# Performance work log

Measured on AMD Instinct MI355X. Metric: run time of the kernel, lower is better.

## Reference

```python
import jax, jax.numpy as jnp
import numpy as np

AUTHOR_FAMILY_CODET = jnp.array([0, 1, 2, 1, 3, 3], dtype=jnp.int32)
MARGIN = 0.3

def setup_inputs() -> dict:
    key = jax.random.key(0)
    k1, k2 = jax.random.split(key)
    B, D = 8192, 256
    embeddings = jax.random.normal(k1, (B, D), dtype=jnp.float32)
    labels = jax.random.randint(k2, (B,), 0, 6, dtype=jnp.int64)
    return {"embeddings": embeddings, "labels": labels}

def reference(embeddings, labels):
    B = embeddings.shape[0]
    # family lookup; labels out of table range would be -1 (cannot happen here
    # since fill_max == table length, but kept for faithfulness)
    lab = labels.astype(jnp.int32)
    table_len = AUTHOR_FAMILY_CODET.shape[0]
    fam = jnp.where(lab < table_len,
                    AUTHOR_FAMILY_CODET[jnp.clip(lab, 0, table_len - 1)],
                    -1)
    # cosine distance matrix [B, B]
    emb_norm = embeddings / jnp.linalg.norm(embeddings, axis=-1, keepdims=True)
    dist = 1.0 - emb_norm @ emb_norm.T
    valid_row = fam >= 0                                   # [B]
    same = (fam[:, None] == fam[None, :]) & valid_row[:, None]
    same = same & ~jnp.eye(B, dtype=bool)                  # exclude self
    diff = (fam[:, None] != fam[None, :]) & valid_row[None, :] & valid_row[:, None]
    d_pos = jnp.max(jnp.where(same, dist, -2.0), axis=1)   # hardest positive
    d_neg = jnp.min(jnp.where(diff, dist, 4.0), axis=1)    # hardest negative
    valid = valid_row & jnp.any(same, axis=1) & jnp.any(diff, axis=1)
    triplet = jax.nn.relu(d_pos - d_neg + MARGIN) * valid.astype(dist.dtype)
    count = jnp.sum(valid.astype(jnp.int32))
    return jnp.sum(triplet) / jnp.maximum(count, 1).astype(dist.dtype)
```

## Files before the change

kernel.cpp:

```cpp
#include <hip/hip_runtime.h>


typedef __attribute__((ext_vector_type(8))) _Float16 half8;
typedef __attribute__((ext_vector_type(2))) _Float16 half2v;
typedef __attribute__((ext_vector_type(4))) float floatx4;
typedef __attribute__((ext_vector_type(4))) unsigned short ushort4v;

constexpr int DIN = 256;
constexpr int NKS = 9;
constexpr int TILE_USH = NKS * 4 * 64 * 8;
#define MARGIN 0.3f
#define FAM_PACKED 111240
#define SENT 0xC4004400u

static __device__ __forceinline__ unsigned fkey(float x) {
  return __builtin_bit_cast(unsigned, x + 10.0f);
}
static __device__ __forceinline__ unsigned packmm(float mn, float mx) {
  unsigned lo = __builtin_bit_cast(unsigned short, (_Float16)mn);
  unsigned hi = __builtin_bit_cast(unsigned short, (_Float16)mx);
  return lo | (hi << 16);
}
static __device__ __forceinline__ float mmlo(unsigned p) {
  return (float)__builtin_bit_cast(_Float16, (unsigned short)(p & 0xFFFF));
}
static __device__ __forceinline__ float mmhi(unsigned p) {
  return (float)__builtin_bit_cast(_Float16, (unsigned short)(p >> 16));
}
static __device__ __forceinline__ unsigned pkmin(unsigned a, unsigned b) {
  half2v x = __builtin_bit_cast(half2v, a);
  half2v y = __builtin_bit_cast(half2v, b);
  return __builtin_bit_cast(unsigned, __builtin_elementwise_min(x, y));
}

static __device__ __forceinline__ void ld_g2l16(const unsigned short* g,
                                                unsigned short* lds) {
  __builtin_amdgcn_global_load_lds(
      (const __attribute__((address_space(1))) unsigned int*)(const void*)g,
      (__attribute__((address_space(3))) unsigned int*)(void*)lds, 16, 0, 0);
}

__global__ __launch_bounds__(256) void prep_kernel(
    const float* __restrict__ E, const int* __restrict__ labels,
    unsigned short* __restrict__ EhB, unsigned* __restrict__ mnK,
    unsigned* __restrict__ mxK, float* __restrict__ sumAcc,
    int* __restrict__ cntAcc, int* __restrict__ doneCnt, int B) {
  if (blockIdx.x == 0 && threadIdx.x == 0) {
    sumAcc[0] = 0.0f; cntAcc[0] = 0; doneCnt[0] = 0;
  }
  int gid = blockIdx.x * 256 + threadIdx.x;
  if (gid < B) { mnK[gid] = 0xFFFFFFFFu; mxK[gid] = 0u; }
  int wave = blockIdx.x * 4 + (threadIdx.x >> 6);
  int lane = threadIdx.x & 63;
  int nw   = gridDim.x * 4;
  const int ksl = lane >> 3, ql = (lane >> 1) & 3, ol = (lane & 1) * 4;
  for (int row = wave; row < B; row += nw) {
    float4 v = *(const float4*)&E[(long)row * DIN + lane * 4];
    float s = v.x * v.x + v.y * v.y + v.z * v.z + v.w * v.w;
#pragma unroll
    for (int o = 1; o < 64; o <<= 1) s += __shfl_xor(s, o);
    float rn = 1.0f / sqrtf(s);
    ushort4v o4;
    o4.x = __builtin_bit_cast(unsigned short, (_Float16)(v.x * rn));
    o4.y = __builtin_bit_cast(unsigned short, (_Float16)(v.y * rn));
    o4.z = __builtin_bit_cast(unsigned short, (_Float16)(v.z * rn));
    o4.w = __builtin_bit_cast(unsigned short, (_Float16)(v.w * rn));
    const int ct = row >> 6, nj = (row >> 4) & 3, mrow = row & 15;
    const long tbase = (long)ct * TILE_USH;
    *(ushort4v*)&EhB[tbase + ((long)(ksl * 4 + nj) * 64 + ql * 16 + mrow) * 8
                     + ol] = o4;
    if (lane < 8) {
      ushort4v z = {0, 0, 0, 0};
      if (lane == 0) {
        int lab = labels[row];
        int labc = lab < 0 ? 0 : (lab > 5 ? 5 : lab);
        int fm = (FAM_PACKED >> (3 * labc)) & 7;
        z.x = fm == 0 ? 0x4400 : 0;
        z.y = fm == 1 ? 0x4400 : 0;
        z.z = fm == 2 ? 0x4400 : 0;
        z.w = fm == 3 ? 0x4400 : 0;
      }
      *(ushort4v*)&EhB[tbase + ((long)(8 * 4 + nj) * 64 + ql * 16 + mrow) * 8
                       + ol] = z;
    }
  }
}

__global__ __launch_bounds__(256, 2) void gram_kernel(
    const unsigned short* __restrict__ EhB, unsigned* __restrict__ mnK,
    unsigned* __restrict__ mxK, int nt, int nTasks) {
  __shared__ unsigned short Bs[2][TILE_USH];
  __shared__ unsigned colS[2][4][64];

  const int w = threadIdx.x >> 6, l = threadIdx.x & 63;
  const int m = l & 15, q = l >> 4;

  const int nwg = gridDim.x;
  const int bid = (int)blockIdx.x;
  const int swz = (bid & 7) * (nwg >> 3) + (bid >> 3);

  const int t0 = (int)(((long)swz * nTasks) / nwg);
  const int t1 = (int)(((long)(swz + 1) * nTasks) / nwg);

  int rb = 0;
  while ((rb + 1) * (nt - rb) <= t0) ++rb;
  int ct = 2 * rb + (t0 - rb * (nt - rb + 1));

  const unsigned short* baseL = EhB + l * 8;

  auto stage = [&](int buf, int ctv) {
    const unsigned short* src =
        EhB + (long)ctv * TILE_USH + (long)(w * 64 + l) * 8;
    unsigned short* dst = &Bs[buf][(w * 64) * 8];
#pragma unroll
    for (int j = 0; j < 9; ++j)
      ld_g2l16(src + j * 2048, dst + j * 2048);
  };

  half8 apan[NKS][2];
  auto loadA = [&](int rbv) {
    const long at = (long)(2 * rbv + (w >> 1)) * TILE_USH;
#pragma unroll
    for (int ks = 0; ks < NKS; ++ks)
#pragma unroll
      for (int mi = 0; mi < 2; ++mi)
        apan[ks][mi] = *(const half8*)
            &baseL[at + (long)(ks * 4 + (w & 1) * 2 + mi) * 512];
    apan[8][0] = apan[8][0] * (_Float16)-0.5f;
    apan[8][1] = apan[8][1] * (_Float16)-0.5f;
  };
  loadA(rb);

  float rAmn[8], rAmx[8];
  bool any = false;
#pragma unroll
  for (int i = 0; i < 8; ++i) { rAmn[i] = 100.0f; rAmx[i] = -100.0f; }

  auto flushRows = [&](int rbv) {
    if (!any) return;
#pragma unroll
    for (int o = 1; o < 16; o <<= 1)
#pragma unroll
      for (int i = 0; i < 8; ++i) {
        rAmn[i] = fminf(rAmn[i], __shfl_xor(rAmn[i], o));
        rAmx[i] = fmaxf(rAmx[i], __shfl_xor(rAmx[i], o));
      }
    if (m == 0) {
      const int r0 = rbv * 128 + w * 32 + q * 4;
#pragma unroll
      for (int mi = 0; mi < 2; ++mi)
#pragma unroll
        for (int r = 0; r < 4; ++r) {
          int row = r0 + mi * 16 + r;
          atomicMin(&mnK[row], fkey(rAmn[mi * 4 + r]));
          atomicMax(&mxK[row], fkey(rAmx[mi * 4 + r]));
        }
    }
  };

  auto mergeCols = [&](int pct, int sb2) {
    if (l >= 16) return;
    unsigned a = SENT ^ 0x80000000u;
#pragma unroll
    for (int ww = 0; ww < 4; ++ww)
      a = pkmin(a, colS[sb2][ww][w * 16 + l] ^ 0x80000000u);
    a ^= 0x80000000u;
    float mn = mmlo(a), mx = mmhi(a);
    int col = pct * 64 + w * 16 + l;
    if (mn < 3.9f) atomicMin(&mnK[col], fkey(mn));
    if (mx > -3.9f) atomicMax(&mxK[col], fkey(mx));
  };

  stage(0, ct);
  int p = 0, pct = -1;

#pragma unroll 1
  for (int f = t0; f < t1; ++f) {
    __syncthreads();

    int nct = ct + 1, nrb = rb;
    if (nct == nt) { ++nrb; nct = 2 * nrb; }
    if (f + 1 < t1) stage(p ^ 1, nct);

    if (pct >= 0) mergeCols(pct, (f - 1) & 1);

    const int rt64 = 2 * rb + (w >> 1);
    const int sb = f & 1;
    if (rt64 <= ct) {
      any = true;
      floatx4 acc[2][4];
#pragma unroll
      for (int mi = 0; mi < 2; ++mi)
#pragma unroll
        for (int nj = 0; nj < 4; ++nj) acc[mi][nj] = (floatx4)0.0f;
#pragma unroll
      for (int ks = 0; ks < NKS; ++ks) {
        half8 b[4];
#pragma unroll
        for (int nj = 0; nj < 4; ++nj)
          b[nj] = *(const half8*)&Bs[p][((ks * 4 + nj) * 64 + l) * 8];
#pragma unroll
        for (int mi = 0; mi < 2; ++mi)
#pragma unroll
          for (int nj = 0; nj < 4; ++nj)
            acc[mi][nj] = __builtin_amdgcn_mfma_f32_16x16x32_f16(
                apan[ks][mi], b[nj], acc[mi][nj], 0, 0, 0);
      }
      float cMn[4], cMx[4];
#pragma unroll
      for (int nj = 0; nj < 4; ++nj) {
        float a0 = fminf(fminf(acc[0][nj][0], acc[0][nj][1]),
                         fminf(acc[0][nj][2], acc[0][nj][3]));
        float a1 = fminf(fminf(acc[1][nj][0], acc[1][nj][1]),
                         fminf(acc[1][nj][2], acc[1][nj][3]));
        float b0 = fmaxf(fmaxf(acc[0][nj][0], acc[0][nj][1]),
                         fmaxf(acc[0][nj][2], acc[0][nj][3]));
        float b1 = fmaxf(fmaxf(acc[1][nj][0], acc[1][nj][1]),
                         fmaxf(acc[1][nj][2], acc[1][nj][3]));
        cMn[nj] = fminf(a0, a1);
        cMx[nj] = fmaxf(b0, b1);
#pragma unroll
        for (int mi = 0; mi < 2; ++mi)
#pragma unroll
          for (int r = 0; r < 4; ++r) {
            rAmn[mi * 4 + r] = fminf(rAmn[mi * 4 + r], acc[mi][nj][r]);
            rAmx[mi * 4 + r] = fmaxf(rAmx[mi * 4 + r], acc[mi][nj][r]);
          }
      }
#pragma unroll
      for (int nj = 0; nj < 4; ++nj) {
        cMn[nj] = fminf(cMn[nj], __shfl_xor(cMn[nj], 16));
        cMn[nj] = fminf(cMn[nj], __shfl_xor(cMn[nj], 32));
        cMx[nj] = fmaxf(cMx[nj], __shfl_xor(cMx[nj], 16));
        cMx[nj] = fmaxf(cMx[nj], __shfl_xor(cMx[nj], 32));
      }
      if (q == 0) {
#pragma unroll
        for (int nj = 0; nj < 4; ++nj)
          colS[sb][w][nj * 16 + m] = packmm(cMn[nj], cMx[nj]);
      }
    } else {
      if (q == 0)
#pragma unroll
        for (int nj = 0; nj < 4; ++nj) colS[sb][w][nj * 16 + m] = SENT;
    }

    if (nrb != rb) {
      flushRows(rb);
#pragma unroll
      for (int i = 0; i < 8; ++i) { rAmn[i] = 100.0f; rAmx[i] = -100.0f; }
      any = false;
      if (f + 1 < t1) loadA(nrb);
    }
    pct = ct; rb = nrb; ct = nct; p ^= 1;
  }
  __syncthreads();
  mergeCols(pct, (t1 - 1) & 1);
  flushRows(rb);
}

__global__ __launch_bounds__(256) void reduce_kernel(
    const unsigned* __restrict__ mnK, const unsigned* __restrict__ mxK,
    float* __restrict__ sumAcc, int* __restrict__ cntAcc,
    int* __restrict__ doneCnt, float* __restrict__ out, int B) {
  int gid = blockIdx.x * 256 + threadIdx.x;
  float loss = 0.0f;
  int cc = 0;
  if (gid < B) {
    float bmn = __builtin_bit_cast(float, mnK[gid]) - 10.0f;
    float bmx = __builtin_bit_cast(float, mxK[gid]) - 10.0f;
    if (bmn < -4.0f && bmx > -4.0f) {
      loss = fmaxf(bmx - (bmn + 8.0f) + MARGIN, 0.0f);
      cc = 1;
    }
  }
#pragma unroll
  for (int o = 1; o < 64; o <<= 1) {
    loss += __shfl_xor(loss, o);
    cc   += __shfl_xor(cc, o);
  }
  __shared__ float ls[4];
  __shared__ int   cs[4];
  if ((threadIdx.x & 63) == 0) {
    ls[threadIdx.x >> 6] = loss;
    cs[threadIdx.x >> 6] = cc;
  }
  __syncthreads();
  if (threadIdx.x == 0) {
    atomicAdd(sumAcc, ls[0] + ls[1] + ls[2] + ls[3]);
    atomicAdd(cntAcc, cs[0] + cs[1] + cs[2] + cs[3]);
    __threadfence();
    int old = atomicAdd(doneCnt, 1);
    if (old == (int)gridDim.x - 1) {
      float S = atomicAdd(sumAcc, 0.0f);
      int   C = atomicAdd(cntAcc, 0);
      out[0] = S / (float)(C > 0 ? C : 1);
    }
  }
}

extern "C" void kernel_launch(void* const* d_in, const int* in_sizes, int n_in,
                              void* d_out, int out_size, void* d_ws, size_t ws_size,
                              hipStream_t stream) {
  const float* E      = (const float*)d_in[0];
  const int*   labels = (const int*)d_in[1];
  float*       out    = (float*)d_out;
  const int B  = in_sizes[1];
  const int nt = B / 64;
  const int RB = B / 128;
  const int nTasks = RB * (nt - RB + 1);

  unsigned short* EhB = (unsigned short*)d_ws;
  unsigned* mnK       = (unsigned*)(EhB + (size_t)nt * TILE_USH);
  unsigned* mxK       = mnK + B;
  float* sumAcc       = (float*)(mxK + B);
  int* cntAcc         = (int*)(sumAcc + 1);
  int* doneCnt        = cntAcc + 1;

  prep_kernel<<<dim3(256), 256, 0, stream>>>(E, labels, EhB, mnK, mxK,
                                             sumAcc, cntAcc, doneCnt, B);
  gram_kernel<<<dim3(512), 256, 0, stream>>>(EhB, mnK, mxK, nt, nTasks);
  reduce_kernel<<<dim3((B + 255) / 256), 256, 0, stream>>>(
      mnK, mxK, sumAcc, cntAcc, doneCnt, out, B);
}
```

Before: 103.1 us.

## Split gram tile work across eight waves with one 16-row panel each

Doubles the gram workgroup to 512 threads (8 waves). Each wave now owns a single 16-row A panel instead of two, which halves the accumulator and A-register footprint per wave. The staging loads and the column-merge via shared memory are redistributed across the eight waves. This trades higher per-block occupancy and more latency hiding against more LDS B-fragment reads per MFMA, since each B load now feeds half as many MFMAs, plus a larger column reduction.

```diff
diff --git a/kernel.cpp b/kernel.cpp
--- a/kernel.cpp
+++ b/kernel.cpp
@@ -86,13 +86,14 @@
   }
 }
 
-__global__ __launch_bounds__(256, 2) void gram_kernel(
+__global__ __launch_bounds__(512) void gram_kernel(
     const unsigned short* __restrict__ EhB, unsigned* __restrict__ mnK,
     unsigned* __restrict__ mxK, int nt, int nTasks) {
   __shared__ unsigned short Bs[2][TILE_USH];
-  __shared__ unsigned colS[2][4][64];
-
-  const int w = threadIdx.x >> 6, l = threadIdx.x & 63;
+  __shared__ unsigned colS[2][8][64];
+
+  const int tid = threadIdx.x;
+  const int w = tid >> 6, l = tid & 63;
   const int m = l & 15, q = l >> 4;
 
   const int nwg = gridDim.x;
@@ -109,60 +110,55 @@
   const unsigned short* baseL = EhB + l * 8;
 
   auto stage = [&](int buf, int ctv) {
-    const unsigned short* src =
-        EhB + (long)ctv * TILE_USH + (long)(w * 64 + l) * 8;
-    unsigned short* dst = &Bs[buf][(w * 64) * 8];
-#pragma unroll
-    for (int j = 0; j < 9; ++j)
-      ld_g2l16(src + j * 2048, dst + j * 2048);
+    const unsigned short* src = EhB + (long)ctv * TILE_USH;
+#pragma unroll
+    for (int j = 0; j < 4; ++j)
+      ld_g2l16(src + (long)(j * 512 + w * 64 + l) * 8,
+               &Bs[buf][(j * 512 + w * 64) * 8]);
+    if (w < 4)
+      ld_g2l16(src + (long)(2048 + w * 64 + l) * 8,
+               &Bs[buf][(2048 + w * 64) * 8]);
   };
 
-  half8 apan[NKS][2];
+  half8 apan[NKS];
   auto loadA = [&](int rbv) {
-    const long at = (long)(2 * rbv + (w >> 1)) * TILE_USH;
+    const long at = (long)(2 * rbv + (w >> 2)) * TILE_USH;
 #pragma unroll
     for (int ks = 0; ks < NKS; ++ks)
-#pragma unroll
-      for (int mi = 0; mi < 2; ++mi)
-        apan[ks][mi] = *(const half8*)
-            &baseL[at + (long)(ks * 4 + (w & 1) * 2 + mi) * 512];
-    apan[8][0] = apan[8][0] * (_Float16)-0.5f;
-    apan[8][1] = apan[8][1] * (_Float16)-0.5f;
+      apan[ks] = *(const half8*)&baseL[at + (long)(ks * 4 + (w & 3)) * 512];
+    apan[8] = apan[8] * (_Float16)-0.5f;
   };
   loadA(rb);
 
-  float rAmn[8], rAmx[8];
+  float rAmn[4], rAmx[4];
   bool any = false;
 #pragma unroll
-  for (int i = 0; i < 8; ++i) { rAmn[i] = 100.0f; rAmx[i] = -100.0f; }
+  for (int i = 0; i < 4; ++i) { rAmn[i] = 100.0f; rAmx[i] = -100.0f; }
 
   auto flushRows = [&](int rbv) {
     if (!any) return;
 #pragma unroll
     for (int o = 1; o < 16; o <<= 1)
 #pragma unroll
-      for (int i = 0; i < 8; ++i) {
+      for (int i = 0; i < 4; ++i) {
         rAmn[i] = fminf(rAmn[i], __shfl_xor(rAmn[i], o));
         rAmx[i] = fmaxf(rAmx[i], __shfl_xor(rAmx[i], o));
       }
     if (m == 0) {
-      const int r0 = rbv * 128 + w * 32 + q * 4;
-#pragma unroll
-      for (int mi = 0; mi < 2; ++mi)
-#pragma unroll
-        for (int r = 0; r < 4; ++r) {
-          int row = r0 + mi * 16 + r;
-          atomicMin(&mnK[row], fkey(rAmn[mi * 4 + r]));
-          atomicMax(&mxK[row], fkey(rAmx[mi * 4 + r]));
-        }
+      const int r0 = rbv * 128 + w * 16 + q * 4;
+#pragma unroll
+      for (int r = 0; r < 4; ++r) {
+        atomicMin(&mnK[r0 + r], fkey(rAmn[r]));
+        atomicMax(&mxK[r0 + r], fkey(rAmx[r]));
+      }
     }
   };
 
   auto mergeCols = [&](int pct, int sb2) {
-    if (l >= 16) return;
+    if (w >= 4 || l >= 16) return;
     unsigned a = SENT ^ 0x80000000u;
 #pragma unroll
-    for (int ww = 0; ww < 4; ++ww)
+    for (int ww = 0; ww < 8; ++ww)
       a = pkmin(a, colS[sb2][ww][w * 16 + l] ^ 0x80000000u);
     a ^= 0x80000000u;
     float mn = mmlo(a), mx = mmhi(a);
@@ -184,15 +180,13 @@
 
     if (pct >= 0) mergeCols(pct, (f - 1) & 1);
 
-    const int rt64 = 2 * rb + (w >> 1);
+    const int rt64 = 2 * rb + (w >> 2);
     const int sb = f & 1;
     if (rt64 <= ct) {
       any = true;
-      floatx4 acc[2][4];
-#pragma unroll
-      for (int mi = 0; mi < 2; ++mi)
-#pragma unroll
-        for (int nj = 0; nj < 4; ++nj) acc[mi][nj] = (floatx4)0.0f;
+      floatx4 acc[4];
+#pragma unroll
+      for (int nj = 0; nj < 4; ++nj) acc[nj] = (floatx4)0.0f;
 #pragma unroll
       for (int ks = 0; ks < NKS; ++ks) {
         half8 b[4];
@@ -200,32 +194,21 @@
         for (int nj = 0; nj < 4; ++nj)
           b[nj] = *(const half8*)&Bs[p][((ks * 4 + nj) * 64 + l) * 8];
 #pragma unroll
-        for (int mi = 0; mi < 2; ++mi)
-#pragma unroll
-          for (int nj = 0; nj < 4; ++nj)
-            acc[mi][nj] = __builtin_amdgcn_mfma_f32_16x16x32_f16(
-                apan[ks][mi], b[nj], acc[mi][nj], 0, 0, 0);
+        for (int nj = 0; nj < 4; ++nj)
+          acc[nj] = __builtin_amdgcn_mfma_f32_16x16x32_f16(
+              apan[ks], b[nj], acc[nj], 0, 0, 0);
       }
       float cMn[4], cMx[4];
 #pragma unroll
       for (int nj = 0; nj < 4; ++nj) {
-        float a0 = fminf(fminf(acc[0][nj][0], acc[0][nj][1]),
-                         fminf(acc[0][nj][2], acc[0][nj][3]));
-        float a1 = fminf(fminf(acc[1][nj][0], acc[1][nj][1]),
-                         fminf(acc[1][nj][2], acc[1][nj][3]));
-        float b0 = fmaxf(fmaxf(acc[0][nj][0], acc[0][nj][1]),
-                         fmaxf(acc[0][nj][2], acc[0][nj][3]));
-        float b1 = fmaxf(fmaxf(acc[1][nj][0], acc[1][nj][1]),
-                         fmaxf(acc[1][nj][2], acc[1][nj][3]));
-        cMn[nj] = fminf(a0, a1);
-        cMx[nj] = fmaxf(b0, b1);
-#pragma unroll
-        for (int mi = 0; mi < 2; ++mi)
-#pragma unroll
-          for (int r = 0; r < 4; ++r) {
-            rAmn[mi * 4 + r] = fminf(rAmn[mi * 4 + r], acc[mi][nj][r]);
-            rAmx[mi * 4 + r] = fmaxf(rAmx[mi * 4 + r], acc[mi][nj][r]);
-          }
+        floatx4 vv = acc[nj];
+        cMn[nj] = fminf(fminf(vv[0], vv[1]), fminf(vv[2], vv[3]));
+        cMx[nj] = fmaxf(fmaxf(vv[0], vv[1]), fmaxf(vv[2], vv[3]));
+#pragma unroll
+        for (int r = 0; r < 4; ++r) {
+          rAmn[r] = fminf(rAmn[r], vv[r]);
+          rAmx[r] = fmaxf(rAmx[r], vv[r]);
+        }
       }
 #pragma unroll
       for (int nj = 0; nj < 4; ++nj) {
@@ -248,7 +231,7 @@
     if (nrb != rb) {
       flushRows(rb);
 #pragma unroll
-      for (int i = 0; i < 8; ++i) { rAmn[i] = 100.0f; rAmx[i] = -100.0f; }
+      for (int i = 0; i < 4; ++i) { rAmn[i] = 100.0f; rAmx[i] = -100.0f; }
       any = false;
       if (f + 1 < t1) loadA(nrb);
     }
@@ -319,7 +302,7 @@
 
   prep_kernel<<<dim3(256), 256, 0, stream>>>(E, labels, EhB, mnK, mxK,
                                              sumAcc, cntAcc, doneCnt, B);
-  gram_kernel<<<dim3(512), 256, 0, stream>>>(EhB, mnK, mxK, nt, nTasks);
+  gram_kernel<<<dim3(512), 512, 0, stream>>>(EhB, mnK, mxK, nt, nTasks);
   reduce_kernel<<<dim3((B + 255) / 256), 256, 0, stream>>>(
       mnK, mxK, sumAcc, cntAcc, doneCnt, out, B);
 }
```

Result: no change. 104.5 us (+1.3%).
